# Optimization experiments

Hardware: AMD Instinct MI355X
Metric: run time of the kernel (lower is better)

The kernel has to match this reference:

```python
import jax, jax.numpy as jnp
import numpy as np

BITS = 4
MAXQ = (1 << BITS) - 1          # 15
PACK = 32 // BITS               # 8 values per int32
GROUP = 128
CLIPMIN = 1e-5
CLIPMAX = 1e4


def _unpack_rows(qweight, infeatures):
    # qweight: [in/PACK, out] int32; values packed along the row (infeatures) dim.
    shifts = (jnp.arange(PACK, dtype=jnp.int32) * BITS)[None, :, None]   # [1,PACK,1]
    w = (qweight[:, None, :] >> shifts) & MAXQ                            # [in/PACK, PACK, out]
    return w.reshape(-1, qweight.shape[1])[:infeatures].astype(jnp.float32)


def setup_inputs() -> dict:
    key = jax.random.key(0)
    k1, k2, k3, k4, k5 = jax.random.split(key, 5)
    infeatures, outfeatures, tokens = 4096, 4096, 2048
    num_groups = infeatures // GROUP
    x = jax.random.normal(k1, (tokens, infeatures), dtype=jnp.float32)
    # positive scales, well inside [CLIPMIN, CLIPMAX]
    scales = jax.random.uniform(k2, (num_groups, outfeatures), dtype=jnp.float32,
                                minval=0.005, maxval=0.02)
    # zero points roughly centered in the quant range [0, 15]
    zero_points = jax.random.uniform(k3, (num_groups, outfeatures), dtype=jnp.float32,
                                     minval=0.0, maxval=float(MAXQ))
    bias = jax.random.normal(k4, (outfeatures,), dtype=jnp.float32)
    qweight = jax.random.randint(k5, (infeatures // PACK, outfeatures),
                                 jnp.iinfo(jnp.int32).min, jnp.iinfo(jnp.int32).max,
                                 dtype=jnp.int32)
    return {"x": x, "scales": scales, "zero_points": zero_points,
            "bias": bias, "qweight": qweight}


def reference(x, scales, zero_points, bias, qweight):
    infeatures = x.shape[-1]
    out_f = scales.shape[1]
    num_groups = scales.shape[0]
    w = _unpack_rows(qweight, infeatures)                       # [in, out] fp32 in [0,15]
    s = jnp.clip(scales, CLIPMIN, CLIPMAX)                      # [G, out]
    z = jnp.clip(jnp.round(zero_points), 0.0, float(MAXQ))      # [G, out]
    wg = w.reshape(num_groups, GROUP, out_f)                    # [G, group, out]
    deq = ((wg - z[:, None, :]) * s[:, None, :]).reshape(infeatures, out_f)
    return x @ deq + bias
```

## Files before the change

kernel.cpp:

```cpp
#include <hip/hip_runtime.h>
#include <cstdint>
#include <cstddef>

typedef __attribute__((ext_vector_type(8))) short short8;
typedef __attribute__((ext_vector_type(4))) float floatx4;

typedef __attribute__((address_space(1))) const void gvoid_t;
typedef __attribute__((address_space(3))) void lvoid_t;

__device__ inline short f2bf(float f) {
    unsigned u = __float_as_uint(f);
    u = (u + 0x7FFFu + ((u >> 16) & 1u)) >> 16;
    return (short)u;
}

__global__ __launch_bounds__(256) void convert_x_kernel(
    const float* __restrict__ x, short* __restrict__ xb, long long n)
{
    long long i = ((long long)blockIdx.x * 256 + threadIdx.x) * 8;
    if (i + 8 > n) return;
    const float4* p = (const float4*)(x + i);
    float4 v0 = p[0];
    float4 v1 = p[1];
    short8 h;
    h[0] = f2bf(v0.x); h[1] = f2bf(v0.y); h[2] = f2bf(v0.z); h[3] = f2bf(v0.w);
    h[4] = f2bf(v1.x); h[5] = f2bf(v1.y); h[6] = f2bf(v1.z); h[7] = f2bf(v1.w);
    *(short8*)(xb + i) = h;
}

__global__ __launch_bounds__(256) void dequant_kernel(
    const int* __restrict__ qw, const float* __restrict__ scales,
    const float* __restrict__ zps, short* __restrict__ deqT,
    int N, int K)
{
    __shared__ int lds_q[32 * 65];
    const int t  = threadIdx.x;
    const int n0 = blockIdx.x * 64;
    const int r0 = blockIdx.y * 32;

    #pragma unroll
    for (int v = 0; v < 2; ++v) {
        int idx = t + v * 256;
        int row = idx >> 4;
        int c4  = (idx & 15) * 4;
        const int4 q4 = *(const int4*)(qw + (size_t)(r0 + row) * N + n0 + c4);
        int base = row * 65 + c4;
        lds_q[base + 0] = q4.x;
        lds_q[base + 1] = q4.y;
        lds_q[base + 2] = q4.z;
        lds_q[base + 3] = q4.w;
    }
    __syncthreads();

    const int L  = t & 63;
    const int w  = t >> 6;
    const int rq = L & 31;
    const int hi = L >> 5;
    const int g  = (r0 + rq) >> 4;

    #pragma unroll
    for (int it = 0; it < 8; ++it) {
        const int p  = w * 8 + it;
        const int nl = 2 * p + hi;

        float s = scales[(size_t)g * N + n0 + nl];
        s = fminf(fmaxf(s, 1e-5f), 1e4f);
        float z = rintf(zps[(size_t)g * N + n0 + nl]);
        z = fminf(fmaxf(z, 0.0f), 15.0f);

        const int q = lds_q[rq * 65 + nl];
        short8 h;
        #pragma unroll
        for (int j = 0; j < 8; ++j) {
            float f = (float)((q >> (4 * j)) & 15);
            h[j] = f2bf((f - z) * s);
        }
        *(short8*)(deqT + (size_t)(n0 + nl) * K + (size_t)(r0 + rq) * 8) = h;
    }
}

#define BM 128
#define BN 128
#define BK 64

__global__ __launch_bounds__(256) void gemm_bf16_bt(
    const short* __restrict__ A, const short* __restrict__ Bt,
    const float* __restrict__ bias, float* __restrict__ C,
    int M, int N, int K)
{
    __shared__ __align__(16) short a_lds[BM * BK];
    __shared__ __align__(16) short b_lds[BN * BK];

    const int t  = threadIdx.x;
    const int L  = t & 63;
    const int w  = t >> 6;
    const int m0 = blockIdx.y * BM;
    const int n0 = blockIdx.x * BN;
    const int wm = (w & 1) * 64;
    const int wn = (w >> 1) * 64;

    floatx4 acc[4][4] = {};

    const int sr = L >> 3;
    const int sc = L & 7;
    const int gc = sc ^ sr;
    const short* ag = A  + (size_t)(m0 + w * 8 + sr) * K + gc * 8;
    const short* bg = Bt + (size_t)(n0 + w * 8 + sr) * K + gc * 8;
    short* a_dst = a_lds + (w * 8) * BK;
    short* b_dst = b_lds + (w * 8) * BK;

    for (int kt = 0; kt < K; kt += BK) {
        #pragma unroll
        for (int i = 0; i < 4; ++i) {
            __builtin_amdgcn_global_load_lds(
                (gvoid_t*)(ag + (size_t)i * 32 * K + kt),
                (lvoid_t*)(a_dst + i * 32 * BK), 16, 0, 0);
            __builtin_amdgcn_global_load_lds(
                (gvoid_t*)(bg + (size_t)i * 32 * K + kt),
                (lvoid_t*)(b_dst + i * 32 * BK), 16, 0, 0);
        }
        __syncthreads();

        #pragma unroll
        for (int s = 0; s < 2; ++s) {
            const int p = ((s * 4) + (L >> 4)) ^ (L & 7);
            short8 af[4], bfr[4];
            #pragma unroll
            for (int i = 0; i < 4; ++i)
                af[i] = *(const short8*)(a_lds + (wm + 16 * i + (L & 15)) * BK + p * 8);
            #pragma unroll
            for (int j = 0; j < 4; ++j)
                bfr[j] = *(const short8*)(b_lds + (wn + 16 * j + (L & 15)) * BK + p * 8);
            #pragma unroll
            for (int i = 0; i < 4; ++i) {
                #pragma unroll
                for (int j = 0; j < 4; ++j)
                    acc[i][j] = __builtin_amdgcn_mfma_f32_16x16x32_bf16(
                        af[i], bfr[j], acc[i][j], 0, 0, 0);
            }
        }
        __syncthreads();
    }

    float bv[4];
    #pragma unroll
    for (int j = 0; j < 4; ++j)
        bv[j] = bias[n0 + wn + 16 * j + (L & 15)];
    const int col0 = n0 + wn + (L & 15);
    #pragma unroll
    for (int i = 0; i < 4; ++i) {
        const int row0 = m0 + wm + 16 * i + (L >> 4) * 4;
        #pragma unroll
        for (int r = 0; r < 4; ++r) {
            float* outr = C + (size_t)(row0 + r) * N + col0;
            #pragma unroll
            for (int j = 0; j < 4; ++j)
                outr[16 * j] = acc[i][j][r] + bv[j];
        }
    }
}

extern "C" void kernel_launch(void* const* d_in, const int* in_sizes, int n_in,
                              void* d_out, int out_size, void* d_ws, size_t ws_size,
                              hipStream_t stream)
{
    const float* x      = (const float*)d_in[0];
    const float* scales = (const float*)d_in[1];
    const float* zps    = (const float*)d_in[2];
    const float* bias   = (const float*)d_in[3];
    const int*   qw     = (const int*)d_in[4];

    const int N = in_sizes[3];
    const int G = in_sizes[1] / N;
    const int K = G * 128;
    const int M = in_sizes[0] / K;

    short* xb   = (short*)d_ws;
    short* deqT = xb + (size_t)M * K;
    float* out  = (float*)d_out;

    const long long nx = (long long)M * K;
    convert_x_kernel<<<(int)(nx / 2048), 256, 0, stream>>>(x, xb, nx);
    dequant_kernel<<<dim3(N / 64, K / 256), 256, 0, stream>>>(qw, scales, zps, deqT, N, K);
    gemm_bf16_bt<<<dim3(N / BN, M / BM), 256, 0, stream>>>(xb, deqT, bias, out, M, N, K);
}
```

Baseline: 176.8 us.

## Fuse conversion and dequant launches and double-buffer GEMM LDS tiles

Merges the x-to-bf16 conversion and weight dequantization into one kernel launch that splits the block range between the two jobs, removing one launch and its serialization gap. The GEMM now double-buffers the A/B LDS tiles and issues the next tile's global-to-LDS loads before computing on the current one, dropping one barrier per iteration so memory traffic overlaps with MFMA work. This doubles LDS use per block (64 KB), which can cut occupancy. The single remaining barrier may not order the async LDS writes safely against reads of the other buffer.

```diff
diff --git a/kernel.cpp b/kernel.cpp
--- a/kernel.cpp
+++ b/kernel.cpp
@@ -14,29 +14,31 @@
     return (short)u;
 }
 
-__global__ __launch_bounds__(256) void convert_x_kernel(
-    const float* __restrict__ x, short* __restrict__ xb, long long n)
-{
-    long long i = ((long long)blockIdx.x * 256 + threadIdx.x) * 8;
-    if (i + 8 > n) return;
-    const float4* p = (const float4*)(x + i);
-    float4 v0 = p[0];
-    float4 v1 = p[1];
-    short8 h;
-    h[0] = f2bf(v0.x); h[1] = f2bf(v0.y); h[2] = f2bf(v0.z); h[3] = f2bf(v0.w);
-    h[4] = f2bf(v1.x); h[5] = f2bf(v1.y); h[6] = f2bf(v1.z); h[7] = f2bf(v1.w);
-    *(short8*)(xb + i) = h;
-}
-
-__global__ __launch_bounds__(256) void dequant_kernel(
+__global__ __launch_bounds__(256) void prologue_kernel(
+    const float* __restrict__ x, short* __restrict__ xb, long long nx, int ncvt,
     const int* __restrict__ qw, const float* __restrict__ scales,
     const float* __restrict__ zps, short* __restrict__ deqT,
-    int N, int K)
+    int N, int K, int nbx)
 {
     __shared__ int lds_q[32 * 65];
-    const int t  = threadIdx.x;
-    const int n0 = blockIdx.x * 64;
-    const int r0 = blockIdx.y * 32;
+    const int t = threadIdx.x;
+
+    if ((int)blockIdx.x < ncvt) {
+        long long i = ((long long)blockIdx.x * 256 + t) * 8;
+        if (i + 8 > nx) return;
+        const float4* p = (const float4*)(x + i);
+        float4 v0 = p[0];
+        float4 v1 = p[1];
+        short8 h;
+        h[0] = f2bf(v0.x); h[1] = f2bf(v0.y); h[2] = f2bf(v0.z); h[3] = f2bf(v0.w);
+        h[4] = f2bf(v1.x); h[5] = f2bf(v1.y); h[6] = f2bf(v1.z); h[7] = f2bf(v1.w);
+        *(short8*)(xb + i) = h;
+        return;
+    }
+
+    const int b2 = (int)blockIdx.x - ncvt;
+    const int n0 = (b2 % nbx) * 64;
+    const int r0 = (b2 / nbx) * 32;
 
     #pragma unroll
     for (int v = 0; v < 2; ++v) {
@@ -88,8 +90,8 @@
     const float* __restrict__ bias, float* __restrict__ C,
     int M, int N, int K)
 {
-    __shared__ __align__(16) short a_lds[BM * BK];
-    __shared__ __align__(16) short b_lds[BN * BK];
+    __shared__ __align__(16) short a_lds[2][BM * BK];
+    __shared__ __align__(16) short b_lds[2][BN * BK];
 
     const int t  = threadIdx.x;
     const int L  = t & 63;
@@ -106,31 +108,47 @@
     const int gc = sc ^ sr;
     const short* ag = A  + (size_t)(m0 + w * 8 + sr) * K + gc * 8;
     const short* bg = Bt + (size_t)(n0 + w * 8 + sr) * K + gc * 8;
-    short* a_dst = a_lds + (w * 8) * BK;
-    short* b_dst = b_lds + (w * 8) * BK;
-
-    for (int kt = 0; kt < K; kt += BK) {
-        #pragma unroll
-        for (int i = 0; i < 4; ++i) {
-            __builtin_amdgcn_global_load_lds(
-                (gvoid_t*)(ag + (size_t)i * 32 * K + kt),
-                (lvoid_t*)(a_dst + i * 32 * BK), 16, 0, 0);
-            __builtin_amdgcn_global_load_lds(
-                (gvoid_t*)(bg + (size_t)i * 32 * K + kt),
-                (lvoid_t*)(b_dst + i * 32 * BK), 16, 0, 0);
-        }
+    const int dst = (w * 8) * BK;
+
+    const int NK = K / BK;
+
+    #pragma unroll
+    for (int i = 0; i < 4; ++i) {
+        __builtin_amdgcn_global_load_lds(
+            (gvoid_t*)(ag + (size_t)i * 32 * K),
+            (lvoid_t*)(&a_lds[0][dst + i * 32 * BK]), 16, 0, 0);
+        __builtin_amdgcn_global_load_lds(
+            (gvoid_t*)(bg + (size_t)i * 32 * K),
+            (lvoid_t*)(&b_lds[0][dst + i * 32 * BK]), 16, 0, 0);
+    }
+
+    for (int ti = 0; ti < NK; ++ti) {
+        const int cur = ti & 1;
         __syncthreads();
+
+        if (ti + 1 < NK) {
+            const int kn = (ti + 1) * BK;
+            #pragma unroll
+            for (int i = 0; i < 4; ++i) {
+                __builtin_amdgcn_global_load_lds(
+                    (gvoid_t*)(ag + (size_t)i * 32 * K + kn),
+                    (lvoid_t*)(&a_lds[cur ^ 1][dst + i * 32 * BK]), 16, 0, 0);
+                __builtin_amdgcn_global_load_lds(
+                    (gvoid_t*)(bg + (size_t)i * 32 * K + kn),
+                    (lvoid_t*)(&b_lds[cur ^ 1][dst + i * 32 * BK]), 16, 0, 0);
+            }
+        }
 
         #pragma unroll
         for (int s = 0; s < 2; ++s) {
-            const int p = ((s * 4) + (L >> 4)) ^ (L & 7);
+            const int p = (s * 4 + (L >> 4)) ^ (L & 7);
             short8 af[4], bfr[4];
             #pragma unroll
             for (int i = 0; i < 4; ++i)
-                af[i] = *(const short8*)(a_lds + (wm + 16 * i + (L & 15)) * BK + p * 8);
+                af[i] = *(const short8*)(&a_lds[cur][(wm + 16 * i + (L & 15)) * BK + p * 8]);
             #pragma unroll
             for (int j = 0; j < 4; ++j)
-                bfr[j] = *(const short8*)(b_lds + (wn + 16 * j + (L & 15)) * BK + p * 8);
+                bfr[j] = *(const short8*)(&b_lds[cur][(wn + 16 * j + (L & 15)) * BK + p * 8]);
             #pragma unroll
             for (int i = 0; i < 4; ++i) {
                 #pragma unroll
@@ -139,7 +157,6 @@
                         af[i], bfr[j], acc[i][j], 0, 0, 0);
             }
         }
-        __syncthreads();
     }
 
     float bv[4];
@@ -180,7 +197,11 @@
     float* out  = (float*)d_out;
 
     const long long nx = (long long)M * K;
-    convert_x_kernel<<<(int)(nx / 2048), 256, 0, stream>>>(x, xb, nx);
-    dequant_kernel<<<dim3(N / 64, K / 256), 256, 0, stream>>>(qw, scales, zps, deqT, N, K);
+    const int ncvt = (int)(nx / 2048);
+    const int nbx  = N / 64;
+    const int ndq  = nbx * (K / 256);
+
+    prologue_kernel<<<ncvt + ndq, 256, 0, stream>>>(
+        x, xb, nx, ncvt, qw, scales, zps, deqT, N, K, nbx);
     gemm_bf16_bt<<<dim3(N / BN, M / BM), 256, 0, stream>>>(xb, deqT, bias, out, M, N, K);
 }
```

New measurement: 166.9 us. -5.6%, faster.
